# Kernel tuning notes

Measured on AMD Instinct MI355X. Metric: run time of the kernel, lower is better.

The kernel has to match this reference:

```python
import jax, jax.numpy as jnp
import numpy as np

N = 10000
E = 160000
D_IN = 512
D_OUT = 512


def setup_inputs() -> dict:
    key = jax.random.key(0)
    k1, k2, k3, k4, k5 = jax.random.split(key, 5)
    x = jax.random.normal(k1, (N, D_IN), dtype=jnp.float32)
    edge_index = jax.random.randint(k2, (2, E), 0, N, dtype=jnp.int64)
    edge_attr = jax.random.uniform(k3, (E,), dtype=jnp.float32)
    W = jax.random.normal(k4, (D_IN, D_OUT), dtype=jnp.float32) * 0.05
    b = jax.random.normal(k5, (D_OUT,), dtype=jnp.float32) * 0.05
    return {"x": x, "edge_index": edge_index, "edge_attr": edge_attr, "W": W, "b": b}


def reference(x, edge_index, edge_attr, W, b):
    # PyG GCNConv with normalize=True, add_self_loops=True, edge_weight=edge_attr.
    n = x.shape[0]
    row, col = edge_index[0], edge_index[1]
    # Add self loops with weight 1.0 (fill_value=1.)
    loop = jnp.arange(n, dtype=edge_index.dtype)
    row_f = jnp.concatenate([row, loop])      # [E+N] source nodes
    col_f = jnp.concatenate([col, loop])      # [E+N] target nodes
    ew = jnp.concatenate([edge_attr, jnp.ones((n,), dtype=edge_attr.dtype)])
    # Symmetric normalization: deg computed over target index (col)
    deg = jax.ops.segment_sum(ew, col_f, num_segments=n)
    dinv = jnp.where(deg > 0, jax.lax.rsqrt(deg), 0.0)
    norm = dinv[row_f] * ew * dinv[col_f]     # [E+N]
    # Linear transform (no bias inside lin), then gather-scale-scatter
    h = x @ W                                  # [N, D_OUT]
    msg = h[row_f] * norm[:, None]             # [E+N, D_OUT]
    out = jax.ops.segment_sum(msg, col_f, num_segments=n)
    return out + b
```

## Files before the change

kernel.cpp:

```cpp
#include <hip/hip_runtime.h>

#define NN 10000
#define EE 160000
#define DD 512
#define CAP 128

typedef float floatx4 __attribute__((ext_vector_type(4)));
typedef short short8 __attribute__((ext_vector_type(8)));

#define AS3(p) ((__attribute__((address_space(3))) void*)(p))
#define AS1(p) ((const __attribute__((address_space(1))) void*)(p))

static __device__ __forceinline__ unsigned short f2bf(float f) {
    unsigned int u = __float_as_uint(f);
    unsigned int r = (u + 0x7fffu + ((u >> 16) & 1u)) >> 16;
    return (unsigned short)r;
}
static __device__ __forceinline__ float bflo(unsigned int u) {
    return __uint_as_float(u << 16);
}
static __device__ __forceinline__ float bfhi(unsigned int u) {
    return __uint_as_float(u & 0xffff0000u);
}


#define XB_BLOCKS 5000
#define WT_BLOCKS 256
#define EDGE_BLOCKS 625
#define GM_BLOCKS (157 * 4)

__global__ __launch_bounds__(256) void k_prep_xw(const float* __restrict__ x,
                                                 const float* __restrict__ W,
                                                 unsigned short* __restrict__ xb,
                                                 unsigned short* __restrict__ wtb) {
    const int b = blockIdx.x;
    const int tid = threadIdx.x;
    if (b < XB_BLOCKS) {
        int gid = b * 256 + tid;
        float4 v = *(const float4*)&x[(size_t)gid * 4];
        unsigned int p0 = (unsigned int)f2bf(v.x) | ((unsigned int)f2bf(v.y) << 16);
        unsigned int p1 = (unsigned int)f2bf(v.z) | ((unsigned int)f2bf(v.w) << 16);
        *(uint2*)&xb[(size_t)gid * 4] = make_uint2(p0, p1);
    } else {
        __shared__ float T[32][33];
        int idx = b - XB_BLOCKS;
        int bi = idx & 15;
        int bj = idx >> 4;
        int r0 = tid >> 5;
        int cc = tid & 31;
        #pragma unroll
        for (int k = 0; k < 4; k++) {
            int r = r0 + k * 8;
            T[r][cc] = W[(size_t)(bi * 32 + r) * DD + bj * 32 + cc];
        }
        __syncthreads();
        #pragma unroll
        for (int k = 0; k < 4; k++) {
            int r = r0 + k * 8;
            wtb[(size_t)(bj * 32 + r) * DD + bi * 32 + cc] = f2bf(T[cc][r]);
        }
    }
}


__global__ __launch_bounds__(256) void k_gemm_edge(const unsigned short* __restrict__ xb,
                                                   const unsigned short* __restrict__ wtb,
                                                   unsigned short* __restrict__ hb,
                                                   const int* __restrict__ row,
                                                   const int* __restrict__ col,
                                                   const float* __restrict__ ew,
                                                   float* __restrict__ deg,
                                                   int* __restrict__ cursor,
                                                   uint2* __restrict__ erw) {
    __shared__ unsigned short As[64 * 32];
    __shared__ unsigned short Bs[128 * 32];

    const int tid = threadIdx.x;

    if (blockIdx.x < EDGE_BLOCKS) {
        int e = blockIdx.x * 256 + tid;
        int r = row[e];
        int t = col[e];
        float w = ew[e];
        atomicAdd(&deg[t], w);
        int p = atomicAdd(&cursor[t], 1);
        if (p < CAP) erw[t * CAP + p] = make_uint2((unsigned int)r, __float_as_uint(w));
        return;
    }

    const int bid = blockIdx.x - EDGE_BLOCKS;
    const int wave = tid >> 6;
    const int lane = tid & 63;

    const int bm = (bid >> 2) * 64;
    const int bn = (bid & 3) * 128;

    const int wm = (wave >> 1) * 32;
    const int wn = (wave & 1) * 64;

    const int fm = lane & 15;
    const int kb = (lane >> 4) * 8;

    floatx4 acc[2][4];
    #pragma unroll
    for (int i = 0; i < 2; i++)
        #pragma unroll
        for (int j = 0; j < 4; j++)
            acc[i][j] = (floatx4){0.f, 0.f, 0.f, 0.f};

    const int srow = lane >> 2;
    const int scol = (lane & 3) * 8;

    for (int k0 = 0; k0 < DD; k0 += 32) {
        {
            int r = wave * 16 + srow;
            int gr = bm + r; if (gr > NN - 1) gr = NN - 1;
            __builtin_amdgcn_global_load_lds(AS1(xb + (size_t)gr * DD + k0 + scol),
                                             AS3(&As[wave * 512]), 16, 0, 0);
        }
        #pragma unroll
        for (int cc = 0; cc < 2; cc++) {
            int c = wave + cc * 4;
            int nr = bn + c * 16 + srow;
            __builtin_amdgcn_global_load_lds(AS1(wtb + (size_t)nr * DD + k0 + scol),
                                             AS3(&Bs[c * 512]), 16, 0, 0);
        }
        __syncthreads();

        short8 af[2], bfr[4];
        #pragma unroll
        for (int mi = 0; mi < 2; mi++)
            af[mi] = *(const short8*)&As[(wm + mi * 16 + fm) * 32 + kb];
        #pragma unroll
        for (int ni = 0; ni < 4; ni++)
            bfr[ni] = *(const short8*)&Bs[(wn + ni * 16 + fm) * 32 + kb];

        #pragma unroll
        for (int mi = 0; mi < 2; mi++)
            #pragma unroll
            for (int ni = 0; ni < 4; ni++)
                acc[mi][ni] = __builtin_amdgcn_mfma_f32_16x16x32_bf16(af[mi], bfr[ni], acc[mi][ni], 0, 0, 0);

        __syncthreads();
    }

    #pragma unroll
    for (int mi = 0; mi < 2; mi++) {
        #pragma unroll
        for (int ni = 0; ni < 4; ni++) {
            int colg = bn + wn + ni * 16 + (lane & 15);
            int rbase = bm + wm + mi * 16 + (lane >> 4) * 4;
            #pragma unroll
            for (int j = 0; j < 4; j++) {
                int rg = rbase + j;
                if (rg < NN) hb[(size_t)rg * DD + colg] = f2bf(acc[mi][ni][j]);
            }
        }
    }
}


#define EDGE_FMA2(P, W) \
    acc[0] += bflo(P.x) * W; acc[1] += bfhi(P.x) * W; \
    acc[2] += bflo(P.y) * W; acc[3] += bfhi(P.y) * W;

__global__ __launch_bounds__(128, 8) void k_aggregate(const int* __restrict__ cursor,
                                                      const uint2* __restrict__ erw,
                                                      const unsigned short* __restrict__ hb,
                                                      const float* __restrict__ deg,
                                                      const float* __restrict__ bias,
                                                      float* __restrict__ out) {
    const int h = threadIdx.x >> 6;
    const int t = threadIdx.x & 63;
    const int bid = blockIdx.x;
    const int half = bid & 1;
    const int i = (bid >> 1) * 2 + h;
    const int c = half * 256 + t * 4;

    __shared__ int   s_r[2][CAP];
    __shared__ float s_w[2][CAP];

    int cnt = cursor[i];
    if (cnt > CAP) cnt = CAP;
    const uint2* bkt = erw + (size_t)i * CAP;
    if (t < cnt) {
        uint2 p = bkt[t];
        int r = (int)p.x;
        s_r[h][t] = r;
        s_w[h][t] = __uint_as_float(p.y) * rsqrtf(deg[r] + 1.0f);
    }
    if (t + 64 < cnt) {
        uint2 p = bkt[t + 64];
        int r = (int)p.x;
        s_r[h][t + 64] = r;
        s_w[h][t + 64] = __uint_as_float(p.y) * rsqrtf(deg[r] + 1.0f);
    }

    float dv = rsqrtf(deg[i] + 1.0f);
    uint2 hv = *(const uint2*)&hb[(size_t)i * DD + c];
    float4 bv = *(const float4*)&bias[c];

    __syncthreads();

    float acc[4] = {0.f, 0.f, 0.f, 0.f};

    int j = 0;
    for (; j + 8 <= cnt; j += 8) {
        uint2 p0 = *(const uint2*)&hb[(size_t)s_r[h][j    ] * DD + c];
        uint2 p1 = *(const uint2*)&hb[(size_t)s_r[h][j + 1] * DD + c];
        uint2 p2 = *(const uint2*)&hb[(size_t)s_r[h][j + 2] * DD + c];
        uint2 p3 = *(const uint2*)&hb[(size_t)s_r[h][j + 3] * DD + c];
        uint2 p4 = *(const uint2*)&hb[(size_t)s_r[h][j + 4] * DD + c];
        uint2 p5 = *(const uint2*)&hb[(size_t)s_r[h][j + 5] * DD + c];
        uint2 p6 = *(const uint2*)&hb[(size_t)s_r[h][j + 6] * DD + c];
        uint2 p7 = *(const uint2*)&hb[(size_t)s_r[h][j + 7] * DD + c];
        float w0 = s_w[h][j],     w1 = s_w[h][j + 1], w2 = s_w[h][j + 2], w3 = s_w[h][j + 3];
        float w4 = s_w[h][j + 4], w5 = s_w[h][j + 5], w6 = s_w[h][j + 6], w7 = s_w[h][j + 7];
        EDGE_FMA2(p0, w0) EDGE_FMA2(p1, w1) EDGE_FMA2(p2, w2) EDGE_FMA2(p3, w3)
        EDGE_FMA2(p4, w4) EDGE_FMA2(p5, w5) EDGE_FMA2(p6, w6) EDGE_FMA2(p7, w7)
    }
    for (; j + 4 <= cnt; j += 4) {
        uint2 p0 = *(const uint2*)&hb[(size_t)s_r[h][j    ] * DD + c];
        uint2 p1 = *(const uint2*)&hb[(size_t)s_r[h][j + 1] * DD + c];
        uint2 p2 = *(const uint2*)&hb[(size_t)s_r[h][j + 2] * DD + c];
        uint2 p3 = *(const uint2*)&hb[(size_t)s_r[h][j + 3] * DD + c];
        float w0 = s_w[h][j], w1 = s_w[h][j + 1], w2 = s_w[h][j + 2], w3 = s_w[h][j + 3];
        EDGE_FMA2(p0, w0) EDGE_FMA2(p1, w1) EDGE_FMA2(p2, w2) EDGE_FMA2(p3, w3)
    }
    for (; j < cnt; j++) {
        uint2 p0 = *(const uint2*)&hb[(size_t)s_r[h][j] * DD + c];
        float w0 = s_w[h][j];
        EDGE_FMA2(p0, w0)
    }

    float2 o0, o1;
    o0.x = (acc[0] + bflo(hv.x) * dv) * dv + bv.x;
    o0.y = (acc[1] + bfhi(hv.x) * dv) * dv + bv.y;
    o1.x = (acc[2] + bflo(hv.y) * dv) * dv + bv.z;
    o1.y = (acc[3] + bfhi(hv.y) * dv) * dv + bv.w;
    *(float2*)&out[(size_t)i * DD + c] = o0;
    *(float2*)&out[(size_t)i * DD + c + 2] = o1;
}

extern "C" void kernel_launch(void* const* d_in, const int* in_sizes, int n_in,
                              void* d_out, int out_size, void* d_ws, size_t ws_size,
                              hipStream_t stream) {
    const float* x  = (const float*)d_in[0];
    const int*   ei = (const int*)d_in[1];
    const float* ea = (const float*)d_in[2];
    const float* W  = (const float*)d_in[3];
    const float* b  = (const float*)d_in[4];
    float* out = (float*)d_out;

    char* ws = (char*)d_ws;
    unsigned short* hb   = (unsigned short*)ws;
    unsigned short* xb   = (unsigned short*)(ws + 10240000);
    unsigned short* wtb  = (unsigned short*)(ws + 20480000);
    float* deg    = (float*)(ws + 21004288);
    int*   cursor = (int*)  (ws + 21045248);
    uint2* erw    = (uint2*)(ws + 21086208);

    const int* row = ei;
    const int* col = ei + EE;

    hipMemsetAsync(deg, 0, 81920, stream);

    k_prep_xw<<<XB_BLOCKS + WT_BLOCKS, 256, 0, stream>>>(x, W, xb, wtb);

    k_gemm_edge<<<EDGE_BLOCKS + GM_BLOCKS, 256, 0, stream>>>(xb, wtb, hb, row, col, ea,
                                                             deg, cursor, erw);

    k_aggregate<<<NN, 128, 0, stream>>>(cursor, erw, hb, deg, b, out);
}
```

Baseline: 127.6 us.

## Fuse x bf16 conversion into GEMM, fold memset into prep, split aggregate columns

The separate x-to-bf16 conversion pass is removed. The GEMM now loads fp32 x directly, converts it in registers and stores the bf16 tile to LDS, which avoids writing and re-reading a 10 MB intermediate. The deg/cursor memset is folded into the weight-prep kernel as extra zeroing blocks, saving one launch. The aggregate kernel splits each row into four column quarters with two columns per thread, doubling the block count, and stores pre-shifted row offsets. The trade-offs are that the GEMM A loads become synchronous register loads instead of async global_load_lds, and the aggregate repeats the per-edge metadata loads four times per node.

```diff
diff --git a/kernel.cpp b/kernel.cpp
--- a/kernel.cpp
+++ b/kernel.cpp
@@ -24,28 +24,20 @@
 }
 
 
-#define XB_BLOCKS 5000
 #define WT_BLOCKS 256
+#define ZERO_BLOCKS 20
 #define EDGE_BLOCKS 625
 #define GM_BLOCKS (157 * 4)
 
-__global__ __launch_bounds__(256) void k_prep_xw(const float* __restrict__ x,
-                                                 const float* __restrict__ W,
-                                                 unsigned short* __restrict__ xb,
-                                                 unsigned short* __restrict__ wtb) {
+__global__ __launch_bounds__(256) void k_prep_w(const float* __restrict__ W,
+                                                unsigned short* __restrict__ wtb,
+                                                uint4* __restrict__ zbase) {
     const int b = blockIdx.x;
     const int tid = threadIdx.x;
-    if (b < XB_BLOCKS) {
-        int gid = b * 256 + tid;
-        float4 v = *(const float4*)&x[(size_t)gid * 4];
-        unsigned int p0 = (unsigned int)f2bf(v.x) | ((unsigned int)f2bf(v.y) << 16);
-        unsigned int p1 = (unsigned int)f2bf(v.z) | ((unsigned int)f2bf(v.w) << 16);
-        *(uint2*)&xb[(size_t)gid * 4] = make_uint2(p0, p1);
-    } else {
+    if (b < WT_BLOCKS) {
         __shared__ float T[32][33];
-        int idx = b - XB_BLOCKS;
-        int bi = idx & 15;
-        int bj = idx >> 4;
+        int bi = b & 15;
+        int bj = b >> 4;
         int r0 = tid >> 5;
         int cc = tid & 31;
         #pragma unroll
@@ -59,11 +51,14 @@
             int r = r0 + k * 8;
             wtb[(size_t)(bj * 32 + r) * DD + bi * 32 + cc] = f2bf(T[cc][r]);
         }
-    }
-}
-
-
-__global__ __launch_bounds__(256) void k_gemm_edge(const unsigned short* __restrict__ xb,
+    } else {
+        int idx = (b - WT_BLOCKS) * 256 + tid;
+        zbase[idx] = make_uint4(0u, 0u, 0u, 0u);
+    }
+}
+
+
+__global__ __launch_bounds__(256) void k_gemm_edge(const float* __restrict__ x,
                                                    const unsigned short* __restrict__ wtb,
                                                    unsigned short* __restrict__ hb,
                                                    const int* __restrict__ row,
@@ -111,12 +106,18 @@
     const int srow = lane >> 2;
     const int scol = (lane & 3) * 8;
 
+    int gr = bm + wave * 16 + srow; if (gr > NN - 1) gr = NN - 1;
+    const float* xrow = x + (size_t)gr * DD + scol;
+
     for (int k0 = 0; k0 < DD; k0 += 32) {
         {
-            int r = wave * 16 + srow;
-            int gr = bm + r; if (gr > NN - 1) gr = NN - 1;
-            __builtin_amdgcn_global_load_lds(AS1(xb + (size_t)gr * DD + k0 + scol),
-                                             AS3(&As[wave * 512]), 16, 0, 0);
+            float4 v0 = *(const float4*)(xrow + k0);
+            float4 v1 = *(const float4*)(xrow + k0 + 4);
+            unsigned int u0 = (unsigned int)f2bf(v0.x) | ((unsigned int)f2bf(v0.y) << 16);
+            unsigned int u1 = (unsigned int)f2bf(v0.z) | ((unsigned int)f2bf(v0.w) << 16);
+            unsigned int u2 = (unsigned int)f2bf(v1.x) | ((unsigned int)f2bf(v1.y) << 16);
+            unsigned int u3 = (unsigned int)f2bf(v1.z) | ((unsigned int)f2bf(v1.w) << 16);
+            *(uint4*)&As[(size_t)(wave * 16 + srow) * 32 + scol] = make_uint4(u0, u1, u2, u3);
         }
         #pragma unroll
         for (int cc = 0; cc < 2; cc++) {
@@ -160,9 +161,7 @@
 }
 
 
-#define EDGE_FMA2(P, W) \
-    acc[0] += bflo(P.x) * W; acc[1] += bfhi(P.x) * W; \
-    acc[2] += bflo(P.y) * W; acc[3] += bfhi(P.y) * W;
+#define EDGE_FMA(P, W) a0 += bflo(P) * W; a1 += bfhi(P) * W;
 
 __global__ __launch_bounds__(128, 8) void k_aggregate(const int* __restrict__ cursor,
                                                       const uint2* __restrict__ erw,
@@ -173,9 +172,9 @@
     const int h = threadIdx.x >> 6;
     const int t = threadIdx.x & 63;
     const int bid = blockIdx.x;
-    const int half = bid & 1;
-    const int i = (bid >> 1) * 2 + h;
-    const int c = half * 256 + t * 4;
+    const int q = bid & 3;
+    const int i = (bid >> 2) * 2 + h;
+    const int c = q * 128 + t * 2;
 
     __shared__ int   s_r[2][CAP];
     __shared__ float s_w[2][CAP];
@@ -186,60 +185,57 @@
     if (t < cnt) {
         uint2 p = bkt[t];
         int r = (int)p.x;
-        s_r[h][t] = r;
+        s_r[h][t] = r << 9;
         s_w[h][t] = __uint_as_float(p.y) * rsqrtf(deg[r] + 1.0f);
     }
     if (t + 64 < cnt) {
         uint2 p = bkt[t + 64];
         int r = (int)p.x;
-        s_r[h][t + 64] = r;
+        s_r[h][t + 64] = r << 9;
         s_w[h][t + 64] = __uint_as_float(p.y) * rsqrtf(deg[r] + 1.0f);
     }
 
     float dv = rsqrtf(deg[i] + 1.0f);
-    uint2 hv = *(const uint2*)&hb[(size_t)i * DD + c];
-    float4 bv = *(const float4*)&bias[c];
+    unsigned int hv = *(const unsigned int*)&hb[(size_t)i * DD + c];
+    float2 bv = *(const float2*)&bias[c];
 
     __syncthreads();
 
-    float acc[4] = {0.f, 0.f, 0.f, 0.f};
+    float a0 = 0.f, a1 = 0.f;
 
     int j = 0;
     for (; j + 8 <= cnt; j += 8) {
-        uint2 p0 = *(const uint2*)&hb[(size_t)s_r[h][j    ] * DD + c];
-        uint2 p1 = *(const uint2*)&hb[(size_t)s_r[h][j + 1] * DD + c];
-        uint2 p2 = *(const uint2*)&hb[(size_t)s_r[h][j + 2] * DD + c];
-        uint2 p3 = *(const uint2*)&hb[(size_t)s_r[h][j + 3] * DD + c];
-        uint2 p4 = *(const uint2*)&hb[(size_t)s_r[h][j + 4] * DD + c];
-        uint2 p5 = *(const uint2*)&hb[(size_t)s_r[h][j + 5] * DD + c];
-        uint2 p6 = *(const uint2*)&hb[(size_t)s_r[h][j + 6] * DD + c];
-        uint2 p7 = *(const uint2*)&hb[(size_t)s_r[h][j + 7] * DD + c];
+        unsigned int p0 = *(const unsigned int*)&hb[s_r[h][j    ] + c];
+        unsigned int p1 = *(const unsigned int*)&hb[s_r[h][j + 1] + c];
+        unsigned int p2 = *(const unsigned int*)&hb[s_r[h][j + 2] + c];
+        unsigned int p3 = *(const unsigned int*)&hb[s_r[h][j + 3] + c];
+        unsigned int p4 = *(const unsigned int*)&hb[s_r[h][j + 4] + c];
+        unsigned int p5 = *(const unsigned int*)&hb[s_r[h][j + 5] + c];
+        unsigned int p6 = *(const unsigned int*)&hb[s_r[h][j + 6] + c];
+        unsigned int p7 = *(const unsigned int*)&hb[s_r[h][j + 7] + c];
         float w0 = s_w[h][j],     w1 = s_w[h][j + 1], w2 = s_w[h][j + 2], w3 = s_w[h][j + 3];
         float w4 = s_w[h][j + 4], w5 = s_w[h][j + 5], w6 = s_w[h][j + 6], w7 = s_w[h][j + 7];
-        EDGE_FMA2(p0, w0) EDGE_FMA2(p1, w1) EDGE_FMA2(p2, w2) EDGE_FMA2(p3, w3)
-        EDGE_FMA2(p4, w4) EDGE_FMA2(p5, w5) EDGE_FMA2(p6, w6) EDGE_FMA2(p7, w7)
+        EDGE_FMA(p0, w0) EDGE_FMA(p1, w1) EDGE_FMA(p2, w2) EDGE_FMA(p3, w3)
+        EDGE_FMA(p4, w4) EDGE_FMA(p5, w5) EDGE_FMA(p6, w6) EDGE_FMA(p7, w7)
     }
     for (; j + 4 <= cnt; j += 4) {
-        uint2 p0 = *(const uint2*)&hb[(size_t)s_r[h][j    ] * DD + c];
-        uint2 p1 = *(const uint2*)&hb[(size_t)s_r[h][j + 1] * DD + c];
-        uint2 p2 = *(const uint2*)&hb[(size_t)s_r[h][j + 2] * DD + c];
-        uint2 p3 = *(const uint2*)&hb[(size_t)s_r[h][j + 3] * DD + c];
+        unsigned int p0 = *(const unsigned int*)&hb[s_r[h][j    ] + c];
+        unsigned int p1 = *(const unsigned int*)&hb[s_r[h][j + 1] + c];
+        unsigned int p2 = *(const unsigned int*)&hb[s_r[h][j + 2] + c];
+        unsigned int p3 = *(const unsigned int*)&hb[s_r[h][j + 3] + c];
         float w0 = s_w[h][j], w1 = s_w[h][j + 1], w2 = s_w[h][j + 2], w3 = s_w[h][j + 3];
-        EDGE_FMA2(p0, w0) EDGE_FMA2(p1, w1) EDGE_FMA2(p2, w2) EDGE_FMA2(p3, w3)
+        EDGE_FMA(p0, w0) EDGE_FMA(p1, w1) EDGE_FMA(p2, w2) EDGE_FMA(p3, w3)
     }
     for (; j < cnt; j++) {
-        uint2 p0 = *(const uint2*)&hb[(size_t)s_r[h][j] * DD + c];
+        unsigned int p0 = *(const unsigned int*)&hb[s_r[h][j] + c];
         float w0 = s_w[h][j];
-        EDGE_FMA2(p0, w0)
-    }
-
-    float2 o0, o1;
-    o0.x = (acc[0] + bflo(hv.x) * dv) * dv + bv.x;
-    o0.y = (acc[1] + bfhi(hv.x) * dv) * dv + bv.y;
-    o1.x = (acc[2] + bflo(hv.y) * dv) * dv + bv.z;
-    o1.y = (acc[3] + bfhi(hv.y) * dv) * dv + bv.w;
-    *(float2*)&out[(size_t)i * DD + c] = o0;
-    *(float2*)&out[(size_t)i * DD + c + 2] = o1;
+        EDGE_FMA(p0, w0)
+    }
+
+    float2 o;
+    o.x = (a0 + bflo(hv) * dv) * dv + bv.x;
+    o.y = (a1 + bfhi(hv) * dv) * dv + bv.y;
+    *(float2*)&out[(size_t)i * DD + c] = o;
 }
 
 extern "C" void kernel_launch(void* const* d_in, const int* in_sizes, int n_in,
@@ -254,7 +250,6 @@
 
     char* ws = (char*)d_ws;
     unsigned short* hb   = (unsigned short*)ws;
-    unsigned short* xb   = (unsigned short*)(ws + 10240000);
     unsigned short* wtb  = (unsigned short*)(ws + 20480000);
     float* deg    = (float*)(ws + 21004288);
     int*   cursor = (int*)  (ws + 21045248);
@@ -263,12 +258,10 @@
     const int* row = ei;
     const int* col = ei + EE;
 
-    hipMemsetAsync(deg, 0, 81920, stream);
-
-    k_prep_xw<<<XB_BLOCKS + WT_BLOCKS, 256, 0, stream>>>(x, W, xb, wtb);
-
-    k_gemm_edge<<<EDGE_BLOCKS + GM_BLOCKS, 256, 0, stream>>>(xb, wtb, hb, row, col, ea,
+    k_prep_w<<<WT_BLOCKS + ZERO_BLOCKS, 256, 0, stream>>>(W, wtb, (uint4*)deg);
+
+    k_gemm_edge<<<EDGE_BLOCKS + GM_BLOCKS, 256, 0, stream>>>(x, wtb, hb, row, col, ea,
                                                              deg, cursor, erw);
 
-    k_aggregate<<<NN, 128, 0, stream>>>(cursor, erw, hb, deg, b, out);
-}
+    k_aggregate<<<NN * 2, 128, 0, stream>>>(cursor, erw, hb, deg, b, out);
+}
```

New measurement: 129.0 us. Within noise of the previous version (+1.1%).
